# Kernel optimization log

Hardware: AMD Instinct MI355X
Metric: run time of the kernel (lower is better)

The kernel has to match this reference:

```python
import jax, jax.numpy as jnp
import numpy as np

N = 50000          # nodes
E = 800000         # edges
F_IN = 128         # in_channels
C = 64             # cell channels
NCELLS = 2
STEPS = 4
MULT = 4
N_EDGE_SLOTS = 14  # 2+3+4+5 mixed-op edges per cell
N_OPS = 8          # switch_on
NUM_CLASSES = 40
BN_EPS = 1e-5
GCNII_ALPHA = 0.1


def setup_inputs() -> dict:
    key = jax.random.key(0)
    ks = jax.random.split(key, 20)
    def w(k, shape, fan_in):
        return jax.random.normal(k, shape, dtype=jnp.float32) / np.float32(np.sqrt(fan_in))
    return {
        "x": jax.random.normal(ks[0], (N, F_IN), dtype=jnp.float32),
        "edge_index": jax.random.randint(ks[1], (2, E), 0, N, dtype=jnp.int32),
        "alphas": 0.001 * jax.random.normal(ks[2], (N_EDGE_SLOTS, N_OPS), dtype=jnp.float32),
        "stem_W": w(ks[3], (F_IN, 3 * C), F_IN),
        "pre_W": w(ks[4], (F_IN, C), F_IN),
        "pre0_W0": w(ks[5], (3 * C, C), 3 * C),
        "pre1_W0": w(ks[6], (3 * C, C), 3 * C),
        "pre0_W1": w(ks[7], (3 * C, C), 3 * C),
        "pre1_W1": w(ks[8], (MULT * C, C), MULT * C),
        "W_gcn": w(ks[9], (NCELLS, N_EDGE_SLOTS, C, C), C),
        "W_sage_self": w(ks[10], (NCELLS, N_EDGE_SLOTS, C, C), C),
        "W_sage_nei": w(ks[11], (NCELLS, N_EDGE_SLOTS, C, C), C),
        "W_gin": w(ks[12], (NCELLS, N_EDGE_SLOTS, C, C), C),
        "W_gc1": w(ks[13], (NCELLS, N_EDGE_SLOTS, C, C), C),
        "W_gc2": w(ks[14], (NCELLS, N_EDGE_SLOTS, C, C), C),
        "W_mlp": w(ks[15], (NCELLS, N_EDGE_SLOTS, C, C), C),
        "W_gcnii": w(ks[16], (NCELLS, N_EDGE_SLOTS, C, C), C),
        "cls_W": w(ks[17], (MULT * C + 1, NUM_CLASSES), MULT * C + 1),
        "cls_b": jnp.zeros((NUM_CLASSES,), dtype=jnp.float32),
    }


def reference(x, edge_index, alphas, stem_W, pre_W, pre0_W0, pre1_W0, pre0_W1, pre1_W1,
              W_gcn, W_sage_self, W_sage_nei, W_gin, W_gc1, W_gc2, W_mlp, W_gcnii,
              cls_W, cls_b):
    src, dst = edge_index[0], edge_index[1]
    deg = jax.ops.segment_sum(jnp.ones((E,), jnp.float32), dst, num_segments=N)
    deg = jnp.maximum(deg, 1.0)
    inv_deg = 1.0 / deg
    inv_sqrt = jax.lax.rsqrt(deg)
    edge_norm = (inv_sqrt[src] * inv_sqrt[dst])[:, None]  # [E,1] sym-normalized coeff

    def bn(h):  # batch norm over node axis, no affine (gamma=1, beta=0)
        m = jnp.mean(h, axis=0)
        v = jnp.var(h, axis=0)
        return (h - m) * jax.lax.rsqrt(v + BN_EPS)

    def mlp(xx, W, act):  # Linear(no bias) -> BN -> optional ReLU
        h = bn(xx @ W)
        return jnp.maximum(h, 0.0) if act else h

    relu = lambda t: jnp.maximum(t, 0.0)

    def mixed_op(h, wv, ci, ej, x0):
        # shared message-passing aggregations of h over edge_index
        msg = h[src]                                             # [E,C] gather
        s_sum = jax.ops.segment_sum(msg, dst, num_segments=N)    # sum agg
        s_mean = s_sum * inv_deg[:, None]                        # mean agg
        s_norm = jax.ops.segment_sum(msg * edge_norm, dst, num_segments=N)  # gcn agg
        out = wv[1] * h                                          # skip_connect (wv[0]: none)
        out = out + wv[2] * relu(s_norm @ W_gcn[ci, ej])
        out = out + wv[3] * (h @ W_sage_self[ci, ej] + s_mean @ W_sage_nei[ci, ej])
        out = out + wv[4] * relu((h + s_sum) @ W_gin[ci, ej])
        out = out + wv[5] * (h @ W_gc1[ci, ej] + s_sum @ W_gc2[ci, ej])
        out = out + wv[6] * relu(h @ W_mlp[ci, ej])
        out = out + wv[7] * relu(((1.0 - GCNII_ALPHA) * s_norm + GCNII_ALPHA * x0) @ W_gcnii[ci, ej])
        return out

    wmix = jax.nn.softmax(alphas, axis=-1)  # [14,8], identical across cells

    s0 = s1 = mlp(x, stem_W, act=False)     # stem: MLP([in, 3C], act=None)
    x0 = mlp(x, pre_W, act=True)            # preprocess: MLP([in, C], relu)
    pre_ws = [(pre0_W0, pre1_W0), (pre0_W1, pre1_W1)]
    for ci in range(NCELLS):
        p0, p1 = pre_ws[ci]
        a = mlp(s0, p0, act=True)
        b = mlp(s1, p1, act=True)
        states = [a, b]
        offset = 0
        for _ in range(STEPS):
            s = None
            for j, h in enumerate(states):
                o = mixed_op(h, wmix[offset + j], ci, offset + j, x0)
                s = o if s is None else s + o
            offset += len(states)
            states.append(s)
        out_cell = jnp.concatenate(states[-MULT:], axis=1)  # [N, 4C]
        s0, s1 = s1, out_cell

    pooled = jnp.mean(s1, axis=1, keepdims=True)            # AdaptiveAvgPool1d(1) over channels
    logits = jnp.concatenate([pooled, s1], axis=1) @ cls_W + cls_b
    return logits
```

## Files before the change

### kernel.cpp

```cpp
#include <hip/hip_runtime.h>
#include <stdint.h>

typedef unsigned short u16;
typedef __attribute__((ext_vector_type(8))) short bh8;
typedef __attribute__((ext_vector_type(4))) float f4;

__device__ __forceinline__ float b2f(u16 u){ union{unsigned u; float f;} x; x.u = ((unsigned)u)<<16; return x.f; }
__device__ __forceinline__ u16 f2b(float f){ union{float f; unsigned u;} x; x.f = f; return (u16)((x.u + 0x7fffu + ((x.u>>16)&1u))>>16); }
__device__ __forceinline__ bh8 ld8(const u16* p){ return *reinterpret_cast<const bh8*>(p); }

#define NBK 512

__global__ __launch_bounds__(256) void k_hist(const int* dst, int* hist, int E){
  __shared__ int h[NBK];
  for (int i=threadIdx.x;i<NBK;i+=256) h[i]=0;
  __syncthreads();
  int stride = 256*gridDim.x;
  for (int i = blockIdx.x*256+threadIdx.x; i<E; i+=stride)
    atomicAdd(&h[dst[i]>>7], 1);
  __syncthreads();
  for (int i=threadIdx.x;i<NBK;i+=256){
    int v=h[i]; if (v) atomicAdd(&hist[i], v);
  }
}

__global__ __launch_bounds__(512) void k_scanb(const int* hist, int* bbase, int* bcursor){
  int t = threadIdx.x, lane = t&63, wv = t>>6;
  __shared__ int ws[8];
  int v = hist[t];
  int x = v;
  #pragma unroll
  for (int o=1;o<64;o<<=1){ int u=__shfl_up(x,(unsigned)o,64); if(lane>=o) x+=u; }
  if (lane==63) ws[wv]=x;
  __syncthreads();
  if (t<8){
    int s=ws[t];
    #pragma unroll
    for (int o=1;o<8;o<<=1){ int u=__shfl_up(s,(unsigned)o,8); if (t>=o) s+=u; }
    ws[t]=s;
  }
  __syncthreads();
  int base = (wv==0)?0:ws[wv-1];
  int ex = base + x - v;
  bbase[t]=ex; bcursor[t]=ex;
  if (t==511) bbase[512]=ex+v;
}

__global__ __launch_bounds__(256) void k_bucket(const int* src, const int* dst,
                                                int* bcursor, unsigned* bkt, int E, int nblk){
  __shared__ int h[NBK], base[NBK], lc[NBK];
  int per = (E + nblk - 1)/nblk;
  int e0 = blockIdx.x*per, e1 = min(E, e0+per);
  for (int i=threadIdx.x;i<NBK;i+=256){ h[i]=0; lc[i]=0; }
  __syncthreads();
  for (int e=e0+threadIdx.x; e<e1; e+=256) atomicAdd(&h[dst[e]>>7], 1);
  __syncthreads();
  for (int i=threadIdx.x;i<NBK;i+=256){
    int c=h[i]; base[i] = c ? atomicAdd(&bcursor[i], c) : 0;
  }
  __syncthreads();
  for (int e=e0+threadIdx.x; e<e1; e+=256){
    int d = dst[e];
    int b = d>>7;
    int r = atomicAdd(&lc[b], 1);
    bkt[base[b]+r] = ((unsigned)(d&127)<<25) | (unsigned)src[e];
  }
}

__global__ __launch_bounds__(128) void k_degb(const unsigned* bkt, const int* bbase,
                                              int* off, float* inv_deg, float* invs,
                                              int N, int E){
  int b = blockIdx.x, t = threadIdx.x;
  __shared__ int cnt[128];
  __shared__ int w0tot;
  cnt[t]=0;
  __syncthreads();
  int e0=bbase[b], e1=bbase[b+1];
  for (int e=e0+t; e<e1; e+=128) atomicAdd(&cnt[bkt[e]>>25], 1);
  __syncthreads();
  int v = cnt[t];
  int lane=t&63, wv=t>>6;
  int x=v;
  #pragma unroll
  for (int o=1;o<64;o<<=1){ int u=__shfl_up(x,(unsigned)o,64); if(lane>=o) x+=u; }
  if (t==63) w0tot=x;
  __syncthreads();
  int ex = x - v + (wv ? w0tot : 0);
  int node = b*128 + t;
  if (node < N){
    off[node] = e0 + ex;
    int d = (v<1)?1:v;
    float df=(float)d;
    inv_deg[node]=1.0f/df;
    invs[node]=rsqrtf(df);
  }
  if (b==0 && t==0) off[N]=E;
}

__global__ __launch_bounds__(128) void k_fillb(const unsigned* bkt, const int* bbase,
                                               const int* off, const float* invs,
                                               int2* csr, int N){
  int b = blockIdx.x, t = threadIdx.x;
  __shared__ int cur[128];
  int node = b*128 + t;
  cur[t] = (node < N) ? off[node] : 0;
  __syncthreads();
  int e0=bbase[b], e1=bbase[b+1];
  for (int e=e0+t; e<e1; e+=128){
    unsigned v = bkt[e];
    int i = (int)(v>>25);
    int s = (int)(v & 0x1FFFFFFu);
    int pos = atomicAdd(&cur[i], 1);
    csr[pos] = make_int2(s, __float_as_int(invs[s]));
  }
}

__global__ void k_softmax(const float* alphas, float* wmix){
  int t = threadIdx.x; int r = t >> 3, o = t & 7;
  if (r < 14){
    float v = alphas[r*8+o];
    float m = v;
    #pragma unroll
    for (int d=1; d<8; d<<=1) m = fmaxf(m, __shfl_xor(m, d, 8));
    float e = expf(v - m);
    float s = e;
    #pragma unroll
    for (int d=1; d<8; d<<=1) s += __shfl_xor(s, d, 8);
    wmix[r*8+o] = e / s;
  }
}

__global__ void k_f2b(const float* a, u16* b, int n){
  int i = blockIdx.x*256 + threadIdx.x;
  if (i < n) b[i] = f2b(a[i]);
}

__global__ void k_pack2d(const float* W, u16* Bp, int K, int ncol){
  int i = blockIdx.x*256 + threadIdx.x;
  if (i < K*ncol){
    int k = i / ncol, n = i - k*ncol;
    Bp[(size_t)n*K + k] = f2b(W[i]);
  }
}

struct PackArgs { const float* W[8]; const float* wmix; u16* dst; };
__global__ void k_pack_ops8(PackArgs P){
  int i = blockIdx.x*256 + threadIdx.x;
  if (i >= 28*8*4096) return;
  int slot28 = i >> 15;
  int rem = i & 32767;
  int mat = rem >> 12;
  int e = rem & 4095;
  int k = e >> 6, n = e & 63;
  const float* wm = P.wmix + (slot28 % 14)*8;
  size_t off = (size_t)slot28*4096 + e;
  float v = 0.f;
  switch(mat){
    case 0: v = wm[2]*P.W[0][off]; break;
    case 1: v = wm[3]*P.W[1][off] + wm[5]*P.W[4][off] + ((k==n) ? wm[1] : 0.f); break;
    case 2: v = wm[3]*P.W[2][off]; break;
    case 3: v = wm[4]*P.W[3][off]; break;
    case 4: v = wm[5]*P.W[5][off]; break;
    case 5: v = wm[6]*P.W[6][off]; break;
    case 6: v = 0.9f*wm[7]*P.W[7][off]; break;
    case 7: v = 0.1f*wm[7]*P.W[7][off]; break;
  }
  P.dst[(((size_t)slot28*8 + mat)<<12) + (n<<6) + (((k>>3) ^ (n&7))<<3) + (k&7)] = f2b(v);
}

__global__ void k_pack_cls(const float* W, u16* Bp){
  int i = blockIdx.x*256 + threadIdx.x;
  if (i < 48*256){
    int n = i >> 8, k = i & 255;
    float v = 0.f;
    if (n < 40) v = W[(size_t)(1+k)*40 + n] + W[n] * (1.f/256.f);
    Bp[(size_t)n*256 + k] = f2b(v);
  }
}

template<int NT, int NKB>
__global__ __launch_bounds__(256) void k_gemm(const u16* A, const u16* Bp,
                                              u16* Tb, int Nn, float* Sp){
  const int K = NKB*32;
  const int ldT = NT*16;
  __shared__ float sred[4][NT*16][2];
  int tid = threadIdx.x, wv = tid>>6, lane = tid&63, q = lane>>4, t = lane&15;
  int row0 = blockIdx.x*128 + wv*32;
  f4 acc[2][NT];
  #pragma unroll
  for (int a=0;a<2;a++)
    #pragma unroll
    for (int b=0;b<NT;b++) acc[a][b] = (f4){0.f,0.f,0.f,0.f};
  const u16* arow0 = A + (size_t)(row0 + t)*K + q*8;
  const u16* arow1 = arow0 + (size_t)16*K;
  const u16* brow  = Bp + (size_t)t*K + q*8;
  #pragma unroll
  for (int kb = 0; kb < NKB; ++kb){
    bh8 a0 = ld8(arow0 + kb*32);
    bh8 a1 = ld8(arow1 + kb*32);
    #pragma unroll
    for (int nt=0; nt<NT; ++nt){
      bh8 bf = ld8(brow + (size_t)nt*16*K + kb*32);
      acc[0][nt] = __builtin_amdgcn_mfma_f32_16x16x32_bf16(a0, bf, acc[0][nt], 0, 0, 0);
      acc[1][nt] = __builtin_amdgcn_mfma_f32_16x16x32_bf16(a1, bf, acc[1][nt], 0, 0, 0);
    }
  }
  #pragma unroll
  for (int nt=0;nt<NT;nt++){
    float ps = 0.f, pq = 0.f;
    #pragma unroll
    for (int rt=0;rt<2;rt++)
      #pragma unroll
      for (int r=0;r<4;r++){
        int row = row0 + rt*16 + q*4 + r;
        float v = acc[rt][nt][r];
        if (row < Nn){
          Tb[(size_t)row*ldT + nt*16 + t] = f2b(v);
          ps += v; pq += v*v;
        }
      }
    ps += __shfl_xor(ps, 16, 64); pq += __shfl_xor(pq, 16, 64);
    ps += __shfl_xor(ps, 32, 64); pq += __shfl_xor(pq, 32, 64);
    if (q == 0){ sred[wv][nt*16 + t][0] = ps; sred[wv][nt*16 + t][1] = pq; }
  }
  __syncthreads();
  if (tid < NT*16){
    float s = sred[0][tid][0] + sred[1][tid][0] + sred[2][tid][0] + sred[3][tid][0];
    float qq = sred[0][tid][1] + sred[1][tid][1] + sred[2][tid][1] + sred[3][tid][1];
    float* sp = Sp + (size_t)blockIdx.x*(2*NT*16);
    sp[tid] = s;
    sp[NT*16 + tid] = qq;
  }
}

__global__ __launch_bounds__(256) void k_redstats(const float* Sp, float* S, int ncol, int nb){
  int c2 = blockIdx.x*4 + (threadIdx.x>>6);
  int lane = threadIdx.x & 63;
  if (c2 >= 2*ncol) return;
  int stride = 2*ncol;
  float s = 0.f;
  for (int b = lane; b < nb; b += 64) s += Sp[(size_t)b*stride + c2];
  #pragma unroll
  for (int m=1; m<64; m<<=1) s += __shfl_xor(s, m, 64);
  if (lane == 0){
    int c = (c2 < ncol) ? c2 : (256 + (c2 - ncol));
    S[c] = s;
  }
}

__global__ void k_norm(const u16* Tb, int ldT, int ncols, int Nn, const float* S,
                       u16* out, int rs_out, int relu, float invN){
  int i = blockIdx.x*256 + threadIdx.x;
  int nv = ncols >> 3;
  if (i >= Nn*nv) return;
  int r = i / nv, c8 = (i - r*nv)*8;
  bh8 tv = ld8(Tb + (size_t)r*ldT + c8);
  bh8 ov;
  #pragma unroll
  for (int u=0; u<8; ++u){
    int c = c8 + u;
    float m = S[c]*invN;
    float var = S[256+c]*invN - m*m;
    float xv = (b2f((u16)tv[u]) - m) * rsqrtf(var + 1e-5f);
    if (relu) xv = fmaxf(xv, 0.f);
    ov[u] = (short)f2b(xv);
  }
  *reinterpret_cast<bh8*>(out + (size_t)r*rs_out + c8) = ov;
}

#define ACC4(vv, ww) { \
    float c0 = __uint_as_float((vv).x << 16); \
    float c1 = __uint_as_float((vv).x & 0xffff0000u); \
    float c2 = __uint_as_float((vv).y << 16); \
    float c3 = __uint_as_float((vv).y & 0xffff0000u); \
    s0 += c0; s1 += c1; s2 += c2; s3 += c3; \
    n0 += c0*(ww); n1 += c1*(ww); n2 += c2*(ww); n3 += c3*(ww); }

template<int SHIFT>
__global__ __launch_bounds__(256) void k_aggv(const u16* h, const int* off, const int2* csr,
                                              const float* inv_sqrt, u16* out_sum, u16* out_norm, int Nn){
  int g = blockIdx.x*4 + (threadIdx.x >> 6);
  if (g >= Nn) return;
  int lane = threadIdx.x & 63;
  int sub = lane >> 4;
  int cb = (lane & 15) << 2;
  const u16* hp = h + cb;
  float s0=0.f,s1=0.f,s2=0.f,s3=0.f;
  float n0=0.f,n1=0.f,n2=0.f,n3=0.f;
  int e0 = off[g], e1 = off[g+1];
  int e = e0 + sub;
  for (; e + 12 < e1; e += 16){
    int2 cA = csr[e];
    int2 cB = csr[e+4];
    int2 cC = csr[e+8];
    int2 cD = csr[e+12];
    uint2 vA = *reinterpret_cast<const uint2*>(hp + (((unsigned)cA.x) << SHIFT));
    uint2 vB = *reinterpret_cast<const uint2*>(hp + (((unsigned)cB.x) << SHIFT));
    uint2 vC = *reinterpret_cast<const uint2*>(hp + (((unsigned)cC.x) << SHIFT));
    uint2 vD = *reinterpret_cast<const uint2*>(hp + (((unsigned)cD.x) << SHIFT));
    float wA = __int_as_float(cA.y), wB = __int_as_float(cB.y);
    float wC = __int_as_float(cC.y), wD = __int_as_float(cD.y);
    ACC4(vA, wA)
    ACC4(vB, wB)
    ACC4(vC, wC)
    ACC4(vD, wD)
  }
  for (; e < e1; e += 4){
    int2 cA = csr[e];
    uint2 vA = *reinterpret_cast<const uint2*>(hp + (((unsigned)cA.x) << SHIFT));
    float wA = __int_as_float(cA.y);
    ACC4(vA, wA)
  }
  s0 += __shfl_xor(s0,16,64); s1 += __shfl_xor(s1,16,64);
  s2 += __shfl_xor(s2,16,64); s3 += __shfl_xor(s3,16,64);
  n0 += __shfl_xor(n0,16,64); n1 += __shfl_xor(n1,16,64);
  n2 += __shfl_xor(n2,16,64); n3 += __shfl_xor(n3,16,64);
  s0 += __shfl_xor(s0,32,64); s1 += __shfl_xor(s1,32,64);
  s2 += __shfl_xor(s2,32,64); s3 += __shfl_xor(s3,32,64);
  n0 += __shfl_xor(n0,32,64); n1 += __shfl_xor(n1,32,64);
  n2 += __shfl_xor(n2,32,64); n3 += __shfl_xor(n3,32,64);
  if (sub == 0){
    float ig = inv_sqrt[g];
    uint2 os, on;
    os.x = (uint)f2b(s0) | ((uint)f2b(s1) << 16);
    os.y = (uint)f2b(s2) | ((uint)f2b(s3) << 16);
    on.x = (uint)f2b(n0*ig) | ((uint)f2b(n1*ig) << 16);
    on.y = (uint)f2b(n2*ig) | ((uint)f2b(n3*ig) << 16);
    *reinterpret_cast<uint2*>(out_sum + (size_t)g*64 + cb) = os;
    *reinterpret_cast<uint2*>(out_norm + (size_t)g*64 + cb) = on;
  }
}

#define ACC4AB(va, vb, ww) { \
    float a0 = __uint_as_float((va).x << 16); \
    float a1 = __uint_as_float((va).x & 0xffff0000u); \
    float a2 = __uint_as_float((va).y << 16); \
    float a3 = __uint_as_float((va).y & 0xffff0000u); \
    float b0 = __uint_as_float((vb).x << 16); \
    float b1 = __uint_as_float((vb).x & 0xffff0000u); \
    float b2 = __uint_as_float((vb).y << 16); \
    float b3 = __uint_as_float((vb).y & 0xffff0000u); \
    sa0 += a0; sa1 += a1; sa2 += a2; sa3 += a3; \
    na0 += a0*(ww); na1 += a1*(ww); na2 += a2*(ww); na3 += a3*(ww); \
    sb0 += b0; sb1 += b1; sb2 += b2; sb3 += b3; \
    nb0 += b0*(ww); nb1 += b1*(ww); nb2 += b2*(ww); nb3 += b3*(ww); }

__global__ __launch_bounds__(256) void k_agg2v(const u16* ab, const int* off, const int2* csr,
                                               const float* inv_sqrt,
                                               u16* os0, u16* on0, u16* os1, u16* on1, int Nn){
  int g = blockIdx.x*4 + (threadIdx.x >> 6);
  if (g >= Nn) return;
  int lane = threadIdx.x & 63;
  int sub = lane >> 4;
  int cb = (lane & 15) << 2;
  const u16* hp = ab + cb;
  float sa0=0.f,sa1=0.f,sa2=0.f,sa3=0.f, na0=0.f,na1=0.f,na2=0.f,na3=0.f;
  float sb0=0.f,sb1=0.f,sb2=0.f,sb3=0.f, nb0=0.f,nb1=0.f,nb2=0.f,nb3=0.f;
  int e0 = off[g], e1 = off[g+1];
  int e = e0 + sub;
  for (; e + 12 < e1; e += 16){
    int2 cA = csr[e];
    int2 cB = csr[e+4];
    int2 cC = csr[e+8];
    int2 cD = csr[e+12];
    const u16* rpA = hp + (((unsigned)cA.x) << 7);
    const u16* rpB = hp + (((unsigned)cB.x) << 7);
    const u16* rpC = hp + (((unsigned)cC.x) << 7);
    const u16* rpD = hp + (((unsigned)cD.x) << 7);
    uint2 vaA = *reinterpret_cast<const uint2*>(rpA);
    uint2 vbA = *reinterpret_cast<const uint2*>(rpA + 64);
    uint2 vaB = *reinterpret_cast<const uint2*>(rpB);
    uint2 vbB = *reinterpret_cast<const uint2*>(rpB + 64);
    uint2 vaC = *reinterpret_cast<const uint2*>(rpC);
    uint2 vbC = *reinterpret_cast<const uint2*>(rpC + 64);
    uint2 vaD = *reinterpret_cast<const uint2*>(rpD);
    uint2 vbD = *reinterpret_cast<const uint2*>(rpD + 64);
    float wA = __int_as_float(cA.y), wB = __int_as_float(cB.y);
    float wC = __int_as_float(cC.y), wD = __int_as_float(cD.y);
    ACC4AB(vaA, vbA, wA)
    ACC4AB(vaB, vbB, wB)
    ACC4AB(vaC, vbC, wC)
    ACC4AB(vaD, vbD, wD)
  }
  for (; e < e1; e += 4){
    int2 cA = csr[e];
    const u16* rpA = hp + (((unsigned)cA.x) << 7);
    uint2 vaA = *reinterpret_cast<const uint2*>(rpA);
    uint2 vbA = *reinterpret_cast<const uint2*>(rpA + 64);
    float wA = __int_as_float(cA.y);
    ACC4AB(vaA, vbA, wA)
  }
  #pragma unroll
  for (int m = 16; m <= 32; m <<= 1){
    sa0 += __shfl_xor(sa0,m,64); sa1 += __shfl_xor(sa1,m,64);
    sa2 += __shfl_xor(sa2,m,64); sa3 += __shfl_xor(sa3,m,64);
    na0 += __shfl_xor(na0,m,64); na1 += __shfl_xor(na1,m,64);
    na2 += __shfl_xor(na2,m,64); na3 += __shfl_xor(na3,m,64);
    sb0 += __shfl_xor(sb0,m,64); sb1 += __shfl_xor(sb1,m,64);
    sb2 += __shfl_xor(sb2,m,64); sb3 += __shfl_xor(sb3,m,64);
    nb0 += __shfl_xor(nb0,m,64); nb1 += __shfl_xor(nb1,m,64);
    nb2 += __shfl_xor(nb2,m,64); nb3 += __shfl_xor(nb3,m,64);
  }
  if (sub == 0){
    float ig = inv_sqrt[g];
    uint2 v;
    v.x = (uint)f2b(sa0) | ((uint)f2b(sa1) << 16);
    v.y = (uint)f2b(sa2) | ((uint)f2b(sa3) << 16);
    *reinterpret_cast<uint2*>(os0 + (size_t)g*64 + cb) = v;
    v.x = (uint)f2b(na0*ig) | ((uint)f2b(na1*ig) << 16);
    v.y = (uint)f2b(na2*ig) | ((uint)f2b(na3*ig) << 16);
    *reinterpret_cast<uint2*>(on0 + (size_t)g*64 + cb) = v;
    v.x = (uint)f2b(sb0) | ((uint)f2b(sb1) << 16);
    v.y = (uint)f2b(sb2) | ((uint)f2b(sb3) << 16);
    *reinterpret_cast<uint2*>(os1 + (size_t)g*64 + cb) = v;
    v.x = (uint)f2b(nb0*ig) | ((uint)f2b(nb1*ig) << 16);
    v.y = (uint)f2b(nb2*ig) | ((uint)f2b(nb3*ig) << 16);
    *reinterpret_cast<uint2*>(on1 + (size_t)g*64 + cb) = v;
  }
}

struct StepArgs {
  const u16* h[5]; const u16* asum[5]; const u16* anorm[5];
  int rs[5]; int slot[5]; int J;
  const u16* wpk; const float* inv_deg; const u16* x0;
  u16* out; int rs_out; int Nn;
};

__device__ __forceinline__ void mm8(const bh8 (&af)[2], const u16* wlds, int mat,
                                    int t, int q, f4 (&acc)[4]){
  #pragma unroll
  for (int kb=0;kb<2;kb++)
    #pragma unroll
    for (int nt=0;nt<4;nt++){
      bh8 bf = ld8(wlds + (mat<<12) + ((nt*16+t)<<6) + ((((kb<<2)|q) ^ (t&7))<<3));
      acc[nt] = __builtin_amdgcn_mfma_f32_16x16x32_bf16(af[kb], bf, acc[nt], 0, 0, 0);
    }
}

__global__ __launch_bounds__(512)
void k_step(StepArgs A){
  __shared__ __align__(16) u16 wlds[8*4096];
  int tid = threadIdx.x, wv = tid>>6, lane = tid&63, q = lane>>4, t = lane&15;
  int row0 = blockIdx.x*128 + wv*16;
  int rA = row0 + t;
  int q8 = q*8;
  f4 idg = *reinterpret_cast<const f4*>(A.inv_deg + row0 + q*4);
  const u16* xp = A.x0 + (size_t)rA*64;
  bh8 fx[2];
  fx[0]=ld8(xp+q8); fx[1]=ld8(xp+32+q8);

  f4 oacc[4];
  #pragma unroll
  for (int b=0;b<4;b++) oacc[b] = (f4){0.f,0.f,0.f,0.f};

  uint4* wdst = reinterpret_cast<uint4*>(wlds);
  for (int j = 0; j < A.J; ++j){
    if (j) __syncthreads();
    const uint4* wsrc = reinterpret_cast<const uint4*>(A.wpk) + ((size_t)A.slot[j] << 12);
    #pragma unroll
    for (int i = 0; i < 8; ++i) wdst[tid + i*512] = wsrc[tid + i*512];

    const u16* h = A.h[j]; int rs = A.rs[j];
    const u16* hp = h + (size_t)rA*rs;
    const u16* sp = A.asum[j] + (size_t)rA*64;
    const u16* np = A.anorm[j] + (size_t)rA*64;
    bh8 fh[2], fs[2], fn[2];
    fh[0]=ld8(hp+q8); fh[1]=ld8(hp+32+q8);
    fs[0]=ld8(sp+q8); fs[1]=ld8(sp+32+q8);
    fn[0]=ld8(np+q8); fn[1]=ld8(np+32+q8);

    __syncthreads();

    mm8(fh, wlds, 1, t, q, oacc);
    mm8(fs, wlds, 4, t, q, oacc);
    f4 p[4];
    #pragma unroll
    for (int b=0;b<4;b++) p[b] = (f4){0.f,0.f,0.f,0.f};
    mm8(fh, wlds, 5, t, q, p);
    #pragma unroll
    for (int nt=0;nt<4;nt++)
      #pragma unroll
      for (int r=0;r<4;r++) oacc[nt][r] += fmaxf(p[nt][r], 0.f);
    #pragma unroll
    for (int b=0;b<4;b++) p[b] = (f4){0.f,0.f,0.f,0.f};
    mm8(fh, wlds, 3, t, q, p);
    mm8(fs, wlds, 3, t, q, p);
    #pragma unroll
    for (int nt=0;nt<4;nt++)
      #pragma unroll
      for (int r=0;r<4;r++) oacc[nt][r] += fmaxf(p[nt][r], 0.f);
    #pragma unroll
    for (int b=0;b<4;b++) p[b] = (f4){0.f,0.f,0.f,0.f};
    mm8(fn, wlds, 0, t, q, p);
    #pragma unroll
    for (int nt=0;nt<4;nt++)
      #pragma unroll
      for (int r=0;r<4;r++) oacc[nt][r] += fmaxf(p[nt][r], 0.f);
    #pragma unroll
    for (int b=0;b<4;b++) p[b] = (f4){0.f,0.f,0.f,0.f};
    mm8(fn, wlds, 6, t, q, p);
    mm8(fx, wlds, 7, t, q, p);
    #pragma unroll
    for (int nt=0;nt<4;nt++)
      #pragma unroll
      for (int r=0;r<4;r++) oacc[nt][r] += fmaxf(p[nt][r], 0.f);
    #pragma unroll
    for (int b=0;b<4;b++) p[b] = (f4){0.f,0.f,0.f,0.f};
    mm8(fs, wlds, 2, t, q, p);
    #pragma unroll
    for (int nt=0;nt<4;nt++)
      #pragma unroll
      for (int r=0;r<4;r++) oacc[nt][r] += idg[r]*p[nt][r];
  }

  #pragma unroll
  for (int nt=0;nt<4;nt++)
    #pragma unroll
    for (int r=0;r<4;r++){
      int rr = row0 + q*4 + r;
      if (rr < A.Nn) A.out[(size_t)rr*A.rs_out + nt*16 + t] = f2b(oacc[nt][r]);
    }
}

__global__ __launch_bounds__(256) void k_cls_mm(const u16* A, const u16* Bp,
                                                const float* bvec, float* out, int Nn){
  int tid = threadIdx.x, wv = tid>>6, lane = tid&63, q = lane>>4, t = lane&15;
  int row0 = blockIdx.x*128 + wv*32;
  f4 acc[2][3];
  #pragma unroll
  for (int a=0;a<2;a++)
    #pragma unroll
    for (int b=0;b<3;b++) acc[a][b] = (f4){0.f,0.f,0.f,0.f};
  const u16* arow0 = A + (size_t)(row0 + t)*256 + q*8;
  const u16* arow1 = arow0 + (size_t)16*256;
  const u16* brow  = Bp + (size_t)t*256 + q*8;
  #pragma unroll
  for (int kb = 0; kb < 8; ++kb){
    bh8 a0 = ld8(arow0 + kb*32);
    bh8 a1 = ld8(arow1 + kb*32);
    #pragma unroll
    for (int nt=0; nt<3; ++nt){
      bh8 bf = ld8(brow + (size_t)nt*16*256 + kb*32);
      acc[0][nt] = __builtin_amdgcn_mfma_f32_16x16x32_bf16(a0, bf, acc[0][nt], 0, 0, 0);
      acc[1][nt] = __builtin_amdgcn_mfma_f32_16x16x32_bf16(a1, bf, acc[1][nt], 0, 0, 0);
    }
  }
  #pragma unroll
  for (int rt=0;rt<2;rt++)
    #pragma unroll
    for (int nt=0;nt<3;nt++){
      int col = nt*16 + t;
      #pragma unroll
      for (int r=0;r<4;r++){
        int row = row0 + rt*16 + q*4 + r;
        if (row < Nn && col < 40) out[(size_t)row*40 + col] = acc[rt][nt][r] + bvec[col];
      }
    }
}

extern "C" void kernel_launch(void* const* d_in, const int* in_sizes, int n_in,
                              void* d_out, int out_size, void* d_ws, size_t ws_size,
                              hipStream_t stream){
  (void)n_in; (void)out_size; (void)ws_size;
  const float* x      = (const float*)d_in[0];
  const int*   ei     = (const int*)d_in[1];
  const float* alphas = (const float*)d_in[2];
  const float* stem_W = (const float*)d_in[3];
  const float* pre_W  = (const float*)d_in[4];
  const float* p00    = (const float*)d_in[5];
  const float* p10    = (const float*)d_in[6];
  const float* p01    = (const float*)d_in[7];
  const float* p11    = (const float*)d_in[8];
  const float* clsW = (const float*)d_in[17];
  const float* clsb = (const float*)d_in[18];

  int N = in_sizes[0] / 128;
  int E = in_sizes[1] / 2;
  const int* esrc = ei;
  const int* edst = ei + E;

  char* p = (char*)d_ws;
  auto carve = [&](size_t bytes) -> char* {
    char* r = p; p += (bytes + 255) & ~(size_t)255; return r;
  };
  int*   hist    = (int*)carve((size_t)NBK*4);
  int*   bbase   = (int*)carve((size_t)(NBK+1)*4);
  int*   bcursor = (int*)carve((size_t)NBK*4);
  unsigned* bkt  = (unsigned*)carve((size_t)E*4);
  int*   off     = (int*)carve((size_t)(N+1)*4);
  int2*  csr     = (int2*)carve((size_t)E*8);
  float* inv_deg = (float*)carve((size_t)N*4);
  float* invs    = (float*)carve((size_t)N*4);
  float* wmix    = (float*)carve(14*8*4);
  float* stats   = (float*)carve(512*4);
  float* Sp      = (float*)carve((size_t)512*384*4);
  u16* xb      = (u16*)carve((size_t)N*128*2);
  u16* stem_pk = (u16*)carve((size_t)192*128*2);
  u16* pre_pk  = (u16*)carve((size_t)64*128*2);
  u16* p00_pk  = (u16*)carve((size_t)64*192*2);
  u16* p10_pk  = (u16*)carve((size_t)64*192*2);
  u16* p01_pk  = (u16*)carve((size_t)64*192*2);
  u16* p11_pk  = (u16*)carve((size_t)64*256*2);
  u16* cls_pk  = (u16*)carve((size_t)48*256*2);
  u16* ops_pk  = (u16*)carve((size_t)28*8*4096*2);
  u16* T       = (u16*)carve((size_t)N*192*2);
  u16* stem_o  = (u16*)carve((size_t)N*192*2);
  u16* x0b     = (u16*)carve((size_t)N*64*2);
  u16* ab      = (u16*)carve((size_t)N*128*2);
  u16* oc0     = (u16*)carve((size_t)N*256*2);
  u16* oc1     = (u16*)carve((size_t)N*256*2);
  u16* agg     = (u16*)carve((size_t)5*2*N*64*2);
  carve(262144);

  auto aggS = [&](int j){ return agg + (size_t)j*2*N*64; };
  auto aggN = [&](int j){ return agg + (size_t)j*2*N*64 + (size_t)N*64; };

  int NB = (N + 127)/128;
  int gg = (N + 127)/128;
  int gstep = (N + 127)/128;
  int ag = (N + 3)/4;
  float invN = 1.0f/(float)N;

  hipMemsetAsync(hist, 0, (size_t)NBK*4, stream);
  k_hist<<<256,256,0,stream>>>(edst, hist, E);
  k_scanb<<<1,512,0,stream>>>(hist, bbase, bcursor);
  k_bucket<<<256,256,0,stream>>>(esrc, edst, bcursor, bkt, E, 256);
  k_degb<<<NB,128,0,stream>>>(bkt, bbase, off, inv_deg, invs, N, E);
  k_fillb<<<NB,128,0,stream>>>(bkt, bbase, off, invs, csr, N);

  k_softmax<<<1,128,0,stream>>>(alphas, wmix);
  k_f2b<<<(N*128+255)/256,256,0,stream>>>(x, xb, N*128);
  k_pack2d<<<(128*192+255)/256,256,0,stream>>>(stem_W, stem_pk, 128, 192);
  k_pack2d<<<(128*64+255)/256,256,0,stream>>>(pre_W, pre_pk, 128, 64);
  k_pack2d<<<(192*64+255)/256,256,0,stream>>>(p00, p00_pk, 192, 64);
  k_pack2d<<<(192*64+255)/256,256,0,stream>>>(p10, p10_pk, 192, 64);
  k_pack2d<<<(192*64+255)/256,256,0,stream>>>(p01, p01_pk, 192, 64);
  k_pack2d<<<(256*64+255)/256,256,0,stream>>>(p11, p11_pk, 256, 64);
  k_pack_cls<<<(48*256+255)/256,256,0,stream>>>(clsW, cls_pk);
  {
    PackArgs PA;
    for (int i = 0; i < 8; ++i) PA.W[i] = (const float*)d_in[9+i];
    PA.wmix = wmix; PA.dst = ops_pk;
    k_pack_ops8<<<(28*8*4096+255)/256,256,0,stream>>>(PA);
  }

  auto mlp = [&](const u16* A, int K, const u16* Bp, int ncol, u16* outb, int rs_out, int relu){
    if (ncol == 192)
      hipLaunchKernelGGL(HIP_KERNEL_NAME(k_gemm<12,4>), dim3(gg), dim3(256), 0, stream, A, Bp, T, N, Sp);
    else if (K == 128)
      hipLaunchKernelGGL(HIP_KERNEL_NAME(k_gemm<4,4>), dim3(gg), dim3(256), 0, stream, A, Bp, T, N, Sp);
    else if (K == 192)
      hipLaunchKernelGGL(HIP_KERNEL_NAME(k_gemm<4,6>), dim3(gg), dim3(256), 0, stream, A, Bp, T, N, Sp);
    else
      hipLaunchKernelGGL(HIP_KERNEL_NAME(k_gemm<4,8>), dim3(gg), dim3(256), 0, stream, A, Bp, T, N, Sp);
    k_redstats<<<(2*ncol+3)/4,256,0,stream>>>(Sp, stats, ncol, gg);
    k_norm<<<((N*(ncol>>3))+255)/256,256,0,stream>>>(T, ncol, ncol, N, stats, outb, rs_out, relu, invN);
  };

  mlp(xb, 128, stem_pk, 192, stem_o, 192, 0);
  mlp(xb, 128, pre_pk, 64, x0b, 64, 1);

  u16* ocs[2] = {oc0, oc1};
  const int slotbase[4] = {0, 2, 5, 9};
  for (int ci = 0; ci < 2; ++ci){
    const u16* s1in = (ci == 0) ? stem_o : oc0;
    int Kb   = (ci == 0) ? 192 : 256;
    const u16* pa = (ci == 0) ? p00_pk : p01_pk;
    const u16* pb = (ci == 0) ? p10_pk : p11_pk;
    mlp(stem_o, 192, pa, 64, ab, 128, 1);
    mlp(s1in, Kb, pb, 64, ab + 64, 128, 1);

    u16* oc = ocs[ci];
    const u16* wpk_cell = ops_pk + (size_t)ci*14*8*4096;

    k_agg2v<<<ag,256,0,stream>>>(ab, off, csr, invs,
                                 aggS(0), aggN(0), aggS(1), aggN(1), N);

    const u16* st[5] = { ab, ab + 64, oc + 0, oc + 64, oc + 128 };
    const int strs[5] = {128, 128, 256, 256, 256};
    for (int step = 0; step < 4; ++step){
      StepArgs SA{};
      int J = step + 2;
      for (int j = 0; j < J; ++j){
        SA.h[j] = st[j]; SA.rs[j] = strs[j];
        SA.asum[j] = aggS(j); SA.anorm[j] = aggN(j);
        SA.slot[j] = slotbase[step] + j;
      }
      SA.J = J; SA.wpk = wpk_cell; SA.inv_deg = inv_deg; SA.x0 = x0b;
      SA.out = oc + (size_t)step*64; SA.rs_out = 256; SA.Nn = N;
      k_step<<<gstep,512,0,stream>>>(SA);
      if (step < 3)
        hipLaunchKernelGGL(HIP_KERNEL_NAME(k_aggv<8>), dim3(ag), dim3(256), 0, stream,
                           oc + (size_t)step*64, off, csr, invs, aggS(step+2), aggN(step+2), N);
    }
  }

  k_cls_mm<<<gg,256,0,stream>>>(oc1, cls_pk, clsb, (float*)d_out, N);
}
```

Measured before the change: 826.5 us.

## Widen aggregation gathers to 16-byte loads, two nodes per wave, XCD-aware block swizzle

The neighbour aggregation kernels now assign 32 lanes per node instead of 64. Each lane gathers 8 bf16 channels with a 16-byte load rather than 4 with an 8-byte load, so fewer, wider memory transactions are issued per gathered row. The dual-input aggregation unroll is reduced to two edges per iteration to offset the doubled accumulator register count. An XCD-aware block-index swizzle is applied to the aggregation and step kernels so neighbouring tiles land on the same chiplet for L2 locality, at the cost of higher register pressure and possibly lower occupancy.

Measured after the change: 791.5 us. 1.04x faster.

```diff
diff --git a/kernel.cpp b/kernel.cpp
--- a/kernel.cpp
+++ b/kernel.cpp
@@ -8,6 +8,12 @@
 __device__ __forceinline__ float b2f(u16 u){ union{unsigned u; float f;} x; x.u = ((unsigned)u)<<16; return x.f; }
 __device__ __forceinline__ u16 f2b(float f){ union{float f; unsigned u;} x; x.f = f; return (u16)((x.u + 0x7fffu + ((x.u>>16)&1u))>>16); }
 __device__ __forceinline__ bh8 ld8(const u16* p){ return *reinterpret_cast<const bh8*>(p); }
+
+__device__ __forceinline__ int xcd_swz(int bid, int nwg){
+  int q = nwg >> 3, r = nwg & 7;
+  int x = bid & 7, k = bid >> 3;
+  return (x < r ? x*(q+1) : r*(q+1) + (x - r)*q) + k;
+}
 
 #define NBK 512
 
@@ -268,25 +274,27 @@
   *reinterpret_cast<bh8*>(out + (size_t)r*rs_out + c8) = ov;
 }
 
-#define ACC4(vv, ww) { \
-    float c0 = __uint_as_float((vv).x << 16); \
-    float c1 = __uint_as_float((vv).x & 0xffff0000u); \
-    float c2 = __uint_as_float((vv).y << 16); \
-    float c3 = __uint_as_float((vv).y & 0xffff0000u); \
-    s0 += c0; s1 += c1; s2 += c2; s3 += c3; \
-    n0 += c0*(ww); n1 += c1*(ww); n2 += c2*(ww); n3 += c3*(ww); }
+#define ACC8(vv, ww) { \
+    float c0=__uint_as_float((vv).x<<16), c1=__uint_as_float((vv).x&0xffff0000u); \
+    float c2=__uint_as_float((vv).y<<16), c3=__uint_as_float((vv).y&0xffff0000u); \
+    float c4=__uint_as_float((vv).z<<16), c5=__uint_as_float((vv).z&0xffff0000u); \
+    float c6=__uint_as_float((vv).w<<16), c7=__uint_as_float((vv).w&0xffff0000u); \
+    s0+=c0; s1+=c1; s2+=c2; s3+=c3; s4+=c4; s5+=c5; s6+=c6; s7+=c7; \
+    n0+=c0*(ww); n1+=c1*(ww); n2+=c2*(ww); n3+=c3*(ww); \
+    n4+=c4*(ww); n5+=c5*(ww); n6+=c6*(ww); n7+=c7*(ww); }
 
 template<int SHIFT>
 __global__ __launch_bounds__(256) void k_aggv(const u16* h, const int* off, const int2* csr,
                                               const float* inv_sqrt, u16* out_sum, u16* out_norm, int Nn){
-  int g = blockIdx.x*4 + (threadIdx.x >> 6);
+  int blk = xcd_swz(blockIdx.x, gridDim.x);
+  int g = blk*8 + (threadIdx.x >> 5);
   if (g >= Nn) return;
-  int lane = threadIdx.x & 63;
-  int sub = lane >> 4;
-  int cb = (lane & 15) << 2;
+  int l32 = threadIdx.x & 31;
+  int sub = l32 >> 3;
+  int cb = (l32 & 7) << 3;
   const u16* hp = h + cb;
-  float s0=0.f,s1=0.f,s2=0.f,s3=0.f;
-  float n0=0.f,n1=0.f,n2=0.f,n3=0.f;
+  float s0=0,s1=0,s2=0,s3=0,s4=0,s5=0,s6=0,s7=0;
+  float n0=0,n1=0,n2=0,n3=0,n4=0,n5=0,n6=0,n7=0;
   int e0 = off[g], e1 = off[g+1];
   int e = e0 + sub;
   for (; e + 12 < e1; e += 16){
@@ -294,128 +302,145 @@
     int2 cB = csr[e+4];
     int2 cC = csr[e+8];
     int2 cD = csr[e+12];
-    uint2 vA = *reinterpret_cast<const uint2*>(hp + (((unsigned)cA.x) << SHIFT));
-    uint2 vB = *reinterpret_cast<const uint2*>(hp + (((unsigned)cB.x) << SHIFT));
-    uint2 vC = *reinterpret_cast<const uint2*>(hp + (((unsigned)cC.x) << SHIFT));
-    uint2 vD = *reinterpret_cast<const uint2*>(hp + (((unsigned)cD.x) << SHIFT));
+    uint4 vA = *reinterpret_cast<const uint4*>(hp + (((unsigned)cA.x) << SHIFT));
+    uint4 vB = *reinterpret_cast<const uint4*>(hp + (((unsigned)cB.x) << SHIFT));
+    uint4 vC = *reinterpret_cast<const uint4*>(hp + (((unsigned)cC.x) << SHIFT));
+    uint4 vD = *reinterpret_cast<const uint4*>(hp + (((unsigned)cD.x) << SHIFT));
     float wA = __int_as_float(cA.y), wB = __int_as_float(cB.y);
     float wC = __int_as_float(cC.y), wD = __int_as_float(cD.y);
-    ACC4(vA, wA)
-    ACC4(vB, wB)
-    ACC4(vC, wC)
-    ACC4(vD, wD)
+    ACC8(vA, wA)
+    ACC8(vB, wB)
+    ACC8(vC, wC)
+    ACC8(vD, wD)
   }
   for (; e < e1; e += 4){
     int2 cA = csr[e];
-    uint2 vA = *reinterpret_cast<const uint2*>(hp + (((unsigned)cA.x) << SHIFT));
+    uint4 vA = *reinterpret_cast<const uint4*>(hp + (((unsigned)cA.x) << SHIFT));
     float wA = __int_as_float(cA.y);
-    ACC4(vA, wA)
-  }
-  s0 += __shfl_xor(s0,16,64); s1 += __shfl_xor(s1,16,64);
-  s2 += __shfl_xor(s2,16,64); s3 += __shfl_xor(s3,16,64);
-  n0 += __shfl_xor(n0,16,64); n1 += __shfl_xor(n1,16,64);
-  n2 += __shfl_xor(n2,16,64); n3 += __shfl_xor(n3,16,64);
-  s0 += __shfl_xor(s0,32,64); s1 += __shfl_xor(s1,32,64);
-  s2 += __shfl_xor(s2,32,64); s3 += __shfl_xor(s3,32,64);
-  n0 += __shfl_xor(n0,32,64); n1 += __shfl_xor(n1,32,64);
-  n2 += __shfl_xor(n2,32,64); n3 += __shfl_xor(n3,32,64);
+    ACC8(vA, wA)
+  }
+  #pragma unroll
+  for (int m = 8; m <= 16; m <<= 1){
+    s0 += __shfl_xor(s0,m,64); s1 += __shfl_xor(s1,m,64);
+    s2 += __shfl_xor(s2,m,64); s3 += __shfl_xor(s3,m,64);
+    s4 += __shfl_xor(s4,m,64); s5 += __shfl_xor(s5,m,64);
+    s6 += __shfl_xor(s6,m,64); s7 += __shfl_xor(s7,m,64);
+    n0 += __shfl_xor(n0,m,64); n1 += __shfl_xor(n1,m,64);
+    n2 += __shfl_xor(n2,m,64); n3 += __shfl_xor(n3,m,64);
+    n4 += __shfl_xor(n4,m,64); n5 += __shfl_xor(n5,m,64);
+    n6 += __shfl_xor(n6,m,64); n7 += __shfl_xor(n7,m,64);
+  }
   if (sub == 0){
     float ig = inv_sqrt[g];
-    uint2 os, on;
-    os.x = (uint)f2b(s0) | ((uint)f2b(s1) << 16);
-    os.y = (uint)f2b(s2) | ((uint)f2b(s3) << 16);
-    on.x = (uint)f2b(n0*ig) | ((uint)f2b(n1*ig) << 16);
-    on.y = (uint)f2b(n2*ig) | ((uint)f2b(n3*ig) << 16);
-    *reinterpret_cast<uint2*>(out_sum + (size_t)g*64 + cb) = os;
-    *reinterpret_cast<uint2*>(out_norm + (size_t)g*64 + cb) = on;
-  }
-}
-
-#define ACC4AB(va, vb, ww) { \
-    float a0 = __uint_as_float((va).x << 16); \
-    float a1 = __uint_as_float((va).x & 0xffff0000u); \
-    float a2 = __uint_as_float((va).y << 16); \
-    float a3 = __uint_as_float((va).y & 0xffff0000u); \
-    float b0 = __uint_as_float((vb).x << 16); \
-    float b1 = __uint_as_float((vb).x & 0xffff0000u); \
-    float b2 = __uint_as_float((vb).y << 16); \
-    float b3 = __uint_as_float((vb).y & 0xffff0000u); \
-    sa0 += a0; sa1 += a1; sa2 += a2; sa3 += a3; \
-    na0 += a0*(ww); na1 += a1*(ww); na2 += a2*(ww); na3 += a3*(ww); \
-    sb0 += b0; sb1 += b1; sb2 += b2; sb3 += b3; \
-    nb0 += b0*(ww); nb1 += b1*(ww); nb2 += b2*(ww); nb3 += b3*(ww); }
+    uint4 o;
+    o.x = (uint)f2b(s0) | ((uint)f2b(s1) << 16);
+    o.y = (uint)f2b(s2) | ((uint)f2b(s3) << 16);
+    o.z = (uint)f2b(s4) | ((uint)f2b(s5) << 16);
+    o.w = (uint)f2b(s6) | ((uint)f2b(s7) << 16);
+    *reinterpret_cast<uint4*>(out_sum + (size_t)g*64 + cb) = o;
+    o.x = (uint)f2b(n0*ig) | ((uint)f2b(n1*ig) << 16);
+    o.y = (uint)f2b(n2*ig) | ((uint)f2b(n3*ig) << 16);
+    o.z = (uint)f2b(n4*ig) | ((uint)f2b(n5*ig) << 16);
+    o.w = (uint)f2b(n6*ig) | ((uint)f2b(n7*ig) << 16);
+    *reinterpret_cast<uint4*>(out_norm + (size_t)g*64 + cb) = o;
+  }
+}
+
+#define ACC8AB(va, vb, ww) { \
+    float a0=__uint_as_float((va).x<<16), a1=__uint_as_float((va).x&0xffff0000u); \
+    float a2=__uint_as_float((va).y<<16), a3=__uint_as_float((va).y&0xffff0000u); \
+    float a4=__uint_as_float((va).z<<16), a5=__uint_as_float((va).z&0xffff0000u); \
+    float a6=__uint_as_float((va).w<<16), a7=__uint_as_float((va).w&0xffff0000u); \
+    float b0=__uint_as_float((vb).x<<16), b1=__uint_as_float((vb).x&0xffff0000u); \
+    float b2=__uint_as_float((vb).y<<16), b3=__uint_as_float((vb).y&0xffff0000u); \
+    float b4=__uint_as_float((vb).z<<16), b5=__uint_as_float((vb).z&0xffff0000u); \
+    float b6=__uint_as_float((vb).w<<16), b7=__uint_as_float((vb).w&0xffff0000u); \
+    sa0+=a0; sa1+=a1; sa2+=a2; sa3+=a3; sa4+=a4; sa5+=a5; sa6+=a6; sa7+=a7; \
+    na0+=a0*(ww); na1+=a1*(ww); na2+=a2*(ww); na3+=a3*(ww); \
+    na4+=a4*(ww); na5+=a5*(ww); na6+=a6*(ww); na7+=a7*(ww); \
+    sb0+=b0; sb1+=b1; sb2+=b2; sb3+=b3; sb4+=b4; sb5+=b5; sb6+=b6; sb7+=b7; \
+    nb0+=b0*(ww); nb1+=b1*(ww); nb2+=b2*(ww); nb3+=b3*(ww); \
+    nb4+=b4*(ww); nb5+=b5*(ww); nb6+=b6*(ww); nb7+=b7*(ww); }
 
 __global__ __launch_bounds__(256) void k_agg2v(const u16* ab, const int* off, const int2* csr,
                                                const float* inv_sqrt,
                                                u16* os0, u16* on0, u16* os1, u16* on1, int Nn){
-  int g = blockIdx.x*4 + (threadIdx.x >> 6);
+  int blk = xcd_swz(blockIdx.x, gridDim.x);
+  int g = blk*8 + (threadIdx.x >> 5);
   if (g >= Nn) return;
-  int lane = threadIdx.x & 63;
-  int sub = lane >> 4;
-  int cb = (lane & 15) << 2;
+  int l32 = threadIdx.x & 31;
+  int sub = l32 >> 3;
+  int cb = (l32 & 7) << 3;
   const u16* hp = ab + cb;
-  float sa0=0.f,sa1=0.f,sa2=0.f,sa3=0.f, na0=0.f,na1=0.f,na2=0.f,na3=0.f;
-  float sb0=0.f,sb1=0.f,sb2=0.f,sb3=0.f, nb0=0.f,nb1=0.f,nb2=0.f,nb3=0.f;
+  float sa0=0,sa1=0,sa2=0,sa3=0,sa4=0,sa5=0,sa6=0,sa7=0;
+  float na0=0,na1=0,na2=0,na3=0,na4=0,na5=0,na6=0,na7=0;
+  float sb0=0,sb1=0,sb2=0,sb3=0,sb4=0,sb5=0,sb6=0,sb7=0;
+  float nb0=0,nb1=0,nb2=0,nb3=0,nb4=0,nb5=0,nb6=0,nb7=0;
   int e0 = off[g], e1 = off[g+1];
   int e = e0 + sub;
-  for (; e + 12 < e1; e += 16){
+  for (; e + 4 < e1; e += 8){
     int2 cA = csr[e];
     int2 cB = csr[e+4];
-    int2 cC = csr[e+8];
-    int2 cD = csr[e+12];
     const u16* rpA = hp + (((unsigned)cA.x) << 7);
     const u16* rpB = hp + (((unsigned)cB.x) << 7);
-    const u16* rpC = hp + (((unsigned)cC.x) << 7);
-    const u16* rpD = hp + (((unsigned)cD.x) << 7);
-    uint2 vaA = *reinterpret_cast<const uint2*>(rpA);
-    uint2 vbA = *reinterpret_cast<const uint2*>(rpA + 64);
-    uint2 vaB = *reinterpret_cast<const uint2*>(rpB);
-    uint2 vbB = *reinterpret_cast<const uint2*>(rpB + 64);
-    uint2 vaC = *reinterpret_cast<const uint2*>(rpC);
-    uint2 vbC = *reinterpret_cast<const uint2*>(rpC + 64);
-    uint2 vaD = *reinterpret_cast<const uint2*>(rpD);
-    uint2 vbD = *reinterpret_cast<const uint2*>(rpD + 64);
+    uint4 vaA = *reinterpret_cast<const uint4*>(rpA);
+    uint4 vbA = *reinterpret_cast<const uint4*>(rpA + 64);
+    uint4 vaB = *reinterpret_cast<const uint4*>(rpB);
+    uint4 vbB = *reinterpret_cast<const uint4*>(rpB + 64);
     float wA = __int_as_float(cA.y), wB = __int_as_float(cB.y);
-    float wC = __int_as_float(cC.y), wD = __int_as_float(cD.y);
-    ACC4AB(vaA, vbA, wA)
-    ACC4AB(vaB, vbB, wB)
-    ACC4AB(vaC, vbC, wC)
-    ACC4AB(vaD, vbD, wD)
-  }
-  for (; e < e1; e += 4){
+    ACC8AB(vaA, vbA, wA)
+    ACC8AB(vaB, vbB, wB)
+  }
+  if (e < e1){
     int2 cA = csr[e];
     const u16* rpA = hp + (((unsigned)cA.x) << 7);
-    uint2 vaA = *reinterpret_cast<const uint2*>(rpA);
-    uint2 vbA = *reinterpret_cast<const uint2*>(rpA + 64);
+    uint4 vaA = *reinterpret_cast<const uint4*>(rpA);
+    uint4 vbA = *reinterpret_cast<const uint4*>(rpA + 64);
     float wA = __int_as_float(cA.y);
-    ACC4AB(vaA, vbA, wA)
-  }
-  #pragma unroll
-  for (int m = 16; m <= 32; m <<= 1){
+    ACC8AB(vaA, vbA, wA)
+  }
+  #pragma unroll
+  for (int m = 8; m <= 16; m <<= 1){
     sa0 += __shfl_xor(sa0,m,64); sa1 += __shfl_xor(sa1,m,64);
     sa2 += __shfl_xor(sa2,m,64); sa3 += __shfl_xor(sa3,m,64);
+    sa4 += __shfl_xor(sa4,m,64); sa5 += __shfl_xor(sa5,m,64);
+    sa6 += __shfl_xor(sa6,m,64); sa7 += __shfl_xor(sa7,m,64);
     na0 += __shfl_xor(na0,m,64); na1 += __shfl_xor(na1,m,64);
     na2 += __shfl_xor(na2,m,64); na3 += __shfl_xor(na3,m,64);
+    na4 += __shfl_xor(na4,m,64); na5 += __shfl_xor(na5,m,64);
+    na6 += __shfl_xor(na6,m,64); na7 += __shfl_xor(na7,m,64);
     sb0 += __shfl_xor(sb0,m,64); sb1 += __shfl_xor(sb1,m,64);
     sb2 += __shfl_xor(sb2,m,64); sb3 += __shfl_xor(sb3,m,64);
+    sb4 += __shfl_xor(sb4,m,64); sb5 += __shfl_xor(sb5,m,64);
+    sb6 += __shfl_xor(sb6,m,64); sb7 += __shfl_xor(sb7,m,64);
     nb0 += __shfl_xor(nb0,m,64); nb1 += __shfl_xor(nb1,m,64);
     nb2 += __shfl_xor(nb2,m,64); nb3 += __shfl_xor(nb3,m,64);
+    nb4 += __shfl_xor(nb4,m,64); nb5 += __shfl_xor(nb5,m,64);
+    nb6 += __shfl_xor(nb6,m,64); nb7 += __shfl_xor(nb7,m,64);
   }
   if (sub == 0){
     float ig = inv_sqrt[g];
-    uint2 v;
-    v.x = (uint)f2b(sa0) | ((uint)f2b(sa1) << 16);
-    v.y = (uint)f2b(sa2) | ((uint)f2b(sa3) << 16);
-    *reinterpret_cast<uint2*>(os0 + (size_t)g*64 + cb) = v;
-    v.x = (uint)f2b(na0*ig) | ((uint)f2b(na1*ig) << 16);
-    v.y = (uint)f2b(na2*ig) | ((uint)f2b(na3*ig) << 16);
-    *reinterpret_cast<uint2*>(on0 + (size_t)g*64 + cb) = v;
-    v.x = (uint)f2b(sb0) | ((uint)f2b(sb1) << 16);
-    v.y = (uint)f2b(sb2) | ((uint)f2b(sb3) << 16);
-    *reinterpret_cast<uint2*>(os1 + (size_t)g*64 + cb) = v;
-    v.x = (uint)f2b(nb0*ig) | ((uint)f2b(nb1*ig) << 16);
-    v.y = (uint)f2b(nb2*ig) | ((uint)f2b(nb3*ig) << 16);
-    *reinterpret_cast<uint2*>(on1 + (size_t)g*64 + cb) = v;
+    uint4 o;
+    o.x = (uint)f2b(sa0) | ((uint)f2b(sa1) << 16);
+    o.y = (uint)f2b(sa2) | ((uint)f2b(sa3) << 16);
+    o.z = (uint)f2b(sa4) | ((uint)f2b(sa5) << 16);
+    o.w = (uint)f2b(sa6) | ((uint)f2b(sa7) << 16);
+    *reinterpret_cast<uint4*>(os0 + (size_t)g*64 + cb) = o;
+    o.x = (uint)f2b(na0*ig) | ((uint)f2b(na1*ig) << 16);
+    o.y = (uint)f2b(na2*ig) | ((uint)f2b(na3*ig) << 16);
+    o.z = (uint)f2b(na4*ig) | ((uint)f2b(na5*ig) << 16);
+    o.w = (uint)f2b(na6*ig) | ((uint)f2b(na7*ig) << 16);
+    *reinterpret_cast<uint4*>(on0 + (size_t)g*64 + cb) = o;
+    o.x = (uint)f2b(sb0) | ((uint)f2b(sb1) << 16);
+    o.y = (uint)f2b(sb2) | ((uint)f2b(sb3) << 16);
+    o.z = (uint)f2b(sb4) | ((uint)f2b(sb5) << 16);
+    o.w = (uint)f2b(sb6) | ((uint)f2b(sb7) << 16);
+    *reinterpret_cast<uint4*>(os1 + (size_t)g*64 + cb) = o;
+    o.x = (uint)f2b(nb0*ig) | ((uint)f2b(nb1*ig) << 16);
+    o.y = (uint)f2b(nb2*ig) | ((uint)f2b(nb3*ig) << 16);
+    o.z = (uint)f2b(nb4*ig) | ((uint)f2b(nb5*ig) << 16);
+    o.w = (uint)f2b(nb6*ig) | ((uint)f2b(nb7*ig) << 16);
+    *reinterpret_cast<uint4*>(on1 + (size_t)g*64 + cb) = o;
   }
 }
 
@@ -441,7 +466,8 @@
 void k_step(StepArgs A){
   __shared__ __align__(16) u16 wlds[8*4096];
   int tid = threadIdx.x, wv = tid>>6, lane = tid&63, q = lane>>4, t = lane&15;
-  int row0 = blockIdx.x*128 + wv*16;
+  int blk = xcd_swz(blockIdx.x, gridDim.x);
+  int row0 = blk*128 + wv*16;
   int rA = row0 + t;
   int q8 = q*8;
   f4 idg = *reinterpret_cast<const f4*>(A.inv_deg + row0 + q*4);
@@ -618,7 +644,7 @@
   int NB = (N + 127)/128;
   int gg = (N + 127)/128;
   int gstep = (N + 127)/128;
-  int ag = (N + 3)/4;
+  int ag = (N + 7)/8;
   float invN = 1.0f/(float)N;
 
   hipMemsetAsync(hist, 0, (size_t)NBK*4, stream);
```
